# Kernel tuning notes

Measured on AMD Instinct MI355X. Metric: run time of the kernel, lower is better.

## Reference

```python
import jax, jax.numpy as jnp
import numpy as np

PAD_TOKEN = 1
V_EN = 32000
V_DE = 32000
WORD_DIM = 300
HID = 500
VLAYER = 500


def lstm(x, Wih, Whh, bih, bhh):
    """Single-layer batch-first LSTM, PyTorch gate order (i,f,g,o). x: [B,T,D] -> h: [B,T,H]."""
    xg = jnp.einsum('btd,gd->btg', x, Wih) + bih  # precompute input projections [B,T,4H]
    H = Whh.shape[1]
    B = x.shape[0]

    def step(carry, xg_t):
        h, c = carry
        g = xg_t + h @ Whh.T + bhh
        i, f, gg, o = jnp.split(g, 4, axis=-1)
        c = jax.nn.sigmoid(f) * c + jax.nn.sigmoid(i) * jnp.tanh(gg)
        h = jax.nn.sigmoid(o) * jnp.tanh(c)
        return (h, c), h

    h0 = jnp.zeros((B, H), x.dtype)
    (_, _), hs = jax.lax.scan(step, (h0, h0), jnp.swapaxes(xg, 0, 1))
    return jnp.swapaxes(hs, 0, 1)


def setup_inputs() -> dict:
    key = jax.random.key(0)
    ks = jax.random.split(key, 12)
    B, S, T = 64, 50, 50
    s = 0.05
    inp = {
        'x_de': jax.random.randint(ks[0], (B, S), 0, V_DE),
        'x_en': jax.random.randint(ks[1], (B, T), 0, V_EN),
        'emb_de_w': jax.random.normal(ks[2], (V_DE, WORD_DIM)) * s,
        'emb_en_w': jax.random.normal(ks[3], (V_EN, WORD_DIM)) * s,
        'enc_Wih': jax.random.normal(ks[4], (4 * HID, WORD_DIM)) * s,
        'enc_Whh': jax.random.normal(ks[5], (4 * HID, HID)) * s,
        'enc_bih': jnp.zeros((4 * HID,)),
        'enc_bhh': jnp.zeros((4 * HID,)),
        'dec_Wih': jax.random.normal(ks[6], (4 * HID, WORD_DIM)) * s,
        'dec_Whh': jax.random.normal(ks[7], (4 * HID, HID)) * s,
        'dec_bih': jnp.zeros((4 * HID,)),
        'dec_bhh': jnp.zeros((4 * HID,)),
        'h2e_w': jax.random.normal(ks[8], (VLAYER, 2 * HID)) * s,
        'h2e_b': jnp.zeros((VLAYER,)),
        'e2v_w': jax.random.normal(ks[9], (V_EN, VLAYER)) * s,
        'e2v_b': jnp.zeros((V_EN,)),
    }
    return inp


def reference(x_de, x_en, emb_de_w, emb_en_w,
              enc_Wih, enc_Whh, enc_bih, enc_bhh,
              dec_Wih, dec_Whh, dec_bih, dec_bhh,
              h2e_w, h2e_b, e2v_w, e2v_b):
    emb_de = emb_de_w[x_de]                       # [B,S,D]
    emb_en = emb_en_w[x_en]                       # [B,T,D]
    enc_h = lstm(emb_de, enc_Wih, enc_Whh, enc_bih, enc_bhh)  # [B,S,H]
    dec_h = lstm(emb_en, dec_Wih, dec_Whh, dec_bih, dec_bhh)  # [B,T,H]

    Tm1 = dec_h.shape[1] - 1
    scores = jnp.einsum('bsh,bth->bst', enc_h, dec_h[:, :Tm1])  # [B,S,T']

    # hard attention: categorical sample per (b,t), all timesteps vectorized
    logp_attn = jax.nn.log_softmax(scores, axis=1)               # [B,S,T']
    samples = jax.random.categorical(jax.random.key(42),
                                     jnp.swapaxes(scores, 1, 2), axis=-1)  # [B,T'] int
    context = jnp.take_along_axis(enc_h, samples[:, :, None], axis=1)      # [B,T',H]

    feat = jnp.concatenate([dec_h[:, :Tm1], context], axis=-1)   # [B,T',2H]
    e = jnp.tanh(feat @ h2e_w.T + h2e_b)
    pred = jax.nn.log_softmax(e @ e2v_w.T + e2v_b, axis=-1)      # [B,T',V]

    y = x_en[:, 1:]                                              # [B,T']
    mask = (y != PAD_TOKEN).astype(pred.dtype)
    reward = jnp.take_along_axis(pred, y[:, :, None], axis=-1)[..., 0]  # [B,T']
    cnt = jnp.maximum(mask.sum(0), 1.0)

    loss = -jnp.sum((reward * mask).sum(0) / cnt)

    logp_s = jnp.take_along_axis(jnp.swapaxes(logp_attn, 1, 2),
                                 samples[:, :, None], axis=-1)[..., 0]  # [B,T']
    baseline = jnp.log(1.0 / V_EN)
    adv = jax.lax.stop_gradient(reward - baseline)
    reinforce_loss = -jnp.sum((logp_s * adv * mask).sum(0) / cnt)

    return loss, reinforce_loss
```

## Files before the change

kernel.cpp:

```cpp
#include <hip/hip_runtime.h>
#include <cstdint>

typedef short short8 __attribute__((ext_vector_type(8)));
typedef float f32x4 __attribute__((ext_vector_type(4)));
typedef uint32_t u32x4 __attribute__((ext_vector_type(4)));
typedef unsigned short u16;
typedef unsigned long long u64;

__device__ __forceinline__ u16 f2bf(float f) {
  union { float f; uint32_t u; } v; v.f = f;
  uint32_t u = v.u;
  uint32_t r = (u + 0x7fffu + ((u >> 16) & 1u)) >> 16;
  return (u16)r;
}
__device__ __forceinline__ float bf2f(u16 b) {
  union { uint32_t u; float f; } v; v.u = ((uint32_t)b) << 16; return v.f;
}
__device__ __forceinline__ float sigm(float x) { return 1.f / (1.f + expf(-x)); }
__device__ __forceinline__ float tanh_f(float x) { return 2.f / (1.f + expf(-2.f * x)) - 1.f; }

typedef const __attribute__((address_space(1))) uint32_t glb_u32;
typedef __attribute__((address_space(3))) uint32_t lds_u32;
__device__ __forceinline__ void glds16(const void* g, void* l) {
  __builtin_amdgcn_global_load_lds((glb_u32*)g, (lds_u32*)l, 16, 0, 0);
}

__device__ __forceinline__ void tfround(uint32_t& a, uint32_t& b, int r) {
  a += b; b = (b << r) | (b >> (32 - r)); b ^= a;
}
__device__ __forceinline__ void threefry(uint32_t k0, uint32_t k1, uint32_t& x0, uint32_t& x1) {
  uint32_t k2 = k0 ^ k1 ^ 0x1BD11BDAu;
  x0 += k0; x1 += k1;
  tfround(x0,x1,13); tfround(x0,x1,15); tfround(x0,x1,26); tfround(x0,x1,6);
  x0 += k1; x1 += k2 + 1u;
  tfround(x0,x1,17); tfround(x0,x1,29); tfround(x0,x1,16); tfround(x0,x1,24);
  x0 += k2; x1 += k0 + 2u;
  tfround(x0,x1,13); tfround(x0,x1,15); tfround(x0,x1,26); tfround(x0,x1,6);
  x0 += k0; x1 += k1 + 3u;
  tfround(x0,x1,17); tfround(x0,x1,29); tfround(x0,x1,16); tfround(x0,x1,24);
  x0 += k1; x1 += k2 + 4u;
  tfround(x0,x1,13); tfround(x0,x1,15); tfround(x0,x1,26); tfround(x0,x1,6);
  x0 += k2; x1 += k0 + 5u;
}
__device__ __forceinline__ float gumbel_from_bits(uint32_t bits) {
  float f = __uint_as_float((bits >> 9) | 0x3f800000u) - 1.0f;
  const float tiny = 1.17549435e-38f;
  float u = fmaxf(f + tiny, tiny);
  return -logf(-logf(u));
}

__global__ __launch_bounds__(256) void prep_all(
    const float* eWih, const float* eWhh, const float* ebih, const float* ebhh,
    const float* dWih, const float* dWhh, const float* dbih, const float* dbhh,
    const float* h2e_w, const float* h2e_b, const float* e2v_w,
    u16* wih_p, u16* whh_p, float* bsum, u16* h2e_p, float* h2e_bp,
    u16* e2v_p, u16* hglob, int* bar)
{
  const uint32_t GWIH = 2u*2048u*40u;
  const uint32_t GWHH = 2u*2048u*64u;
  const uint32_t GBS  = 512u;
  const uint32_t GH2E = 512u*128u;
  const uint32_t GH2EB= 64u;
  const uint32_t GE2V = 32000u*64u;
  const uint32_t GHG  = 16384u;
  const uint32_t GBAR = 64u;
  const uint32_t TOT  = GWIH+GWHH+GBS+GH2E+GH2EB+GE2V+GHG+GBAR;
  for (uint32_t i = blockIdx.x*256u + threadIdx.x; i < TOT; i += gridDim.x*256u) {
    uint32_t j = i;
    if (j < GWIH) {
      uint32_t L = j / (2048u*40u), rem = j % (2048u*40u);
      uint32_t p = rem / 40u, kg = rem % 40u;
      uint32_t g = p >> 9, u = p & 511u, k0 = kg*8u;
      short8 o = {0,0,0,0,0,0,0,0}; u16* op = (u16*)&o;
      if (u < 500u) {
        const float* src = (L ? dWih : eWih) + ((size_t)(g*500u+u))*300u + k0;
        if (k0 + 8u <= 300u) {
          float4 a = *(const float4*)src, b = *(const float4*)(src+4);
          op[0]=f2bf(a.x);op[1]=f2bf(a.y);op[2]=f2bf(a.z);op[3]=f2bf(a.w);
          op[4]=f2bf(b.x);op[5]=f2bf(b.y);op[6]=f2bf(b.z);op[7]=f2bf(b.w);
        } else {
          #pragma unroll
          for (int e = 0; e < 8; ++e) if (k0+e < 300u) op[e] = f2bf(src[e]);
        }
      }
      *(short8*)(wih_p + (size_t)j*8) = o; continue;
    }
    j -= GWIH;
    if (j < GWHH) {
      uint32_t L = j / (2048u*64u), rem = j % (2048u*64u);
      uint32_t row = rem >> 6, kg = rem & 63u, k0 = kg*8u;
      uint32_t wg = row >> 7, r2 = row & 127u, g = r2 >> 5, ul = r2 & 31u;
      uint32_t u = wg*32u + ul;
      short8 o = {0,0,0,0,0,0,0,0}; u16* op = (u16*)&o;
      if (u < 500u) {
        const float* src = (L ? dWhh : eWhh) + ((size_t)(g*500u+u))*500u + k0;
        if (k0 + 8u <= 500u) {
          float4 a = *(const float4*)src, b = *(const float4*)(src+4);
          op[0]=f2bf(a.x);op[1]=f2bf(a.y);op[2]=f2bf(a.z);op[3]=f2bf(a.w);
          op[4]=f2bf(b.x);op[5]=f2bf(b.y);op[6]=f2bf(b.z);op[7]=f2bf(b.w);
        } else {
          #pragma unroll
          for (int e = 0; e < 8; ++e) if (k0+e < 500u) op[e] = f2bf(src[e]);
        }
      }
      *(short8*)(whh_p + (size_t)j*8) = o; continue;
    }
    j -= GWHH;
    if (j < GBS) {
      uint32_t L = j >> 8, pg = j & 255u, p0 = pg*8u;
      float arr[8];
      #pragma unroll
      for (int e = 0; e < 8; ++e) {
        uint32_t p = p0 + e, g = p >> 9, u = p & 511u;
        arr[e] = (u < 500u) ? ((L?dbih:ebih)[g*500u+u] + (L?dbhh:ebhh)[g*500u+u]) : 0.f;
      }
      *(float4*)(bsum + (size_t)j*8) = *(float4*)arr;
      *(float4*)(bsum + (size_t)j*8 + 4) = *(float4*)(arr+4);
      continue;
    }
    j -= GBS;
    if (j < GH2E) {
      uint32_t n = j >> 7, kg = j & 127u, k0 = kg*8u;
      short8 o = {0,0,0,0,0,0,0,0}; u16* op = (u16*)&o;
      if (n < 500u) {
        const float* rowp = h2e_w + (size_t)n*1000u;
        if (k0 + 8u <= 500u) {
          float4 a = *(const float4*)(rowp+k0), b = *(const float4*)(rowp+k0+4);
          op[0]=f2bf(a.x);op[1]=f2bf(a.y);op[2]=f2bf(a.z);op[3]=f2bf(a.w);
          op[4]=f2bf(b.x);op[5]=f2bf(b.y);op[6]=f2bf(b.z);op[7]=f2bf(b.w);
        } else if (k0 >= 512u && k0 + 8u <= 1012u) {
          #pragma unroll
          for (int e = 0; e < 8; ++e) op[e] = f2bf(rowp[k0 + e - 12u]);
        } else {
          #pragma unroll
          for (int e = 0; e < 8; ++e) {
            uint32_t k = k0 + e; float v = 0.f;
            if (k < 500u) v = rowp[k];
            else if (k >= 512u && k < 1012u) v = rowp[k - 12u];
            op[e] = f2bf(v);
          }
        }
      }
      *(short8*)(h2e_p + (size_t)j*8) = o; continue;
    }
    j -= GH2E;
    if (j < GH2EB) {
      uint32_t k0 = j*8u;
      float arr[8];
      #pragma unroll
      for (int e = 0; e < 8; ++e) { uint32_t k = k0+e; arr[e] = (k < 500u) ? h2e_b[k] : 0.f; }
      *(float4*)(h2e_bp + (size_t)j*8) = *(float4*)arr;
      *(float4*)(h2e_bp + (size_t)j*8 + 4) = *(float4*)(arr+4);
      continue;
    }
    j -= GH2EB;
    if (j < GE2V) {
      uint32_t n = j >> 6, kg = j & 63u, k0 = kg*8u;
      short8 o = {0,0,0,0,0,0,0,0}; u16* op = (u16*)&o;
      const float* src = e2v_w + (size_t)n*500u + k0;
      if (k0 + 8u <= 500u) {
        float4 a = *(const float4*)src, b = *(const float4*)(src+4);
        op[0]=f2bf(a.x);op[1]=f2bf(a.y);op[2]=f2bf(a.z);op[3]=f2bf(a.w);
        op[4]=f2bf(b.x);op[5]=f2bf(b.y);op[6]=f2bf(b.z);op[7]=f2bf(b.w);
      } else {
        #pragma unroll
        for (int e = 0; e < 8; ++e) if (k0+e < 500u) op[e] = f2bf(src[e]);
      }
      *(short8*)(e2v_p + (size_t)j*8) = o; continue;
    }
    j -= GE2V;
    if (j < GHG) { short8 z = {0,0,0,0,0,0,0,0}; *(short8*)(hglob + (size_t)j*8) = z; continue; }
    j -= GHG;
    if (j < GBAR) bar[j] = 0;
  }
}

__global__ __launch_bounds__(256, 1) void lstm_kernel(
    const u16* xg , const u16* whh_p,
    u16* hglob , float* h_out , int* bar)
{
  const int wg = blockIdx.x;
  const int lstm = wg >> 4;
  const int wgl = wg & 15;
  const int tid = threadIdx.x;
  const int wid = tid >> 6;
  const int lane = tid & 63;

  __shared__ u16 hbuf[64 * 512];
  __shared__ float pre[4][64][34];
  __shared__ u16 hsh[64 * 32];

  short8 wf[2][16];
  {
    const u16* wbase = whh_p + ((size_t)lstm*2048 + wgl*128 + wid*32) * 512;
    #pragma unroll
    for (int nt = 0; nt < 2; ++nt)
      #pragma unroll
      for (int kk = 0; kk < 16; ++kk) {
        int row = nt*16 + (lane & 15);
        int k = kk*32 + (lane >> 4)*8;
        wf[nt][kk] = *(const short8*)(wbase + (size_t)row*512 + k);
      }
  }

  float c[8];
  #pragma unroll
  for (int q = 0; q < 8; ++q) c[q] = 0.f;

  int* mybar = bar + lstm*32;
  const int ug = wgl*32 + (tid & 31);
  const u16* xgl = xg + ((size_t)lstm*3200)*2048;

  float xr[4][8];
  #pragma unroll
  for (int q = 0; q < 8; ++q) {
    int b = q*8 + (tid >> 5);
    size_t xrow = ((size_t)(b*50 + 0))*2048;
    #pragma unroll
    for (int g = 0; g < 4; ++g) xr[g][q] = bf2f(xgl[xrow + g*512 + ug]);
  }

  #pragma unroll 1
  for (int t = 0; t < 50; ++t) {
    const int cur = t & 1;
    {
      u32x4 sv[16];
      const char* sbase = (const char*)(hglob + ((size_t)(cur*2 + lstm))*64*512);
      #pragma unroll
      for (int i = 0; i < 16; ++i) {
        const void* p = sbase + (size_t)(i*256 + tid)*16;
        asm volatile("global_load_dwordx4 %0, %1, off sc0 sc1" : "=v"(sv[i]) : "v"(p));
      }
      asm volatile("s_waitcnt vmcnt(0)" ::: "memory");
      __builtin_amdgcn_sched_barrier(0);
      #pragma unroll
      for (int i = 0; i < 16; ++i) {
        int chunk = i*256 + tid;
        int row = chunk >> 6, col16 = chunk & 63;
        int byte = row*1024 + ((col16*16) ^ ((row & 7) << 4));
        *(u32x4*)((char*)hbuf + byte) = sv[i];
      }
    }
    __syncthreads();

    f32x4 zero = {0.f, 0.f, 0.f, 0.f};
    f32x4 acc[4][2];
    #pragma unroll
    for (int m = 0; m < 4; ++m) { acc[m][0] = zero; acc[m][1] = zero; }

    #pragma unroll
    for (int kk = 0; kk < 16; ++kk) {
      short8 af[4];
      #pragma unroll
      for (int m = 0; m < 4; ++m) {
        int row = m*16 + (lane & 15);
        int byte = row*1024 + ((kk*64 + (lane >> 4)*16) ^ ((row & 7) << 4));
        af[m] = *(const short8*)((const char*)hbuf + byte);
      }
      #pragma unroll
      for (int m = 0; m < 4; ++m) {
        acc[m][0] = __builtin_amdgcn_mfma_f32_16x16x32_bf16(af[m], wf[0][kk], acc[m][0], 0, 0, 0);
        acc[m][1] = __builtin_amdgcn_mfma_f32_16x16x32_bf16(af[m], wf[1][kk], acc[m][1], 0, 0, 0);
      }
    }

    #pragma unroll
    for (int m = 0; m < 4; ++m)
      #pragma unroll
      for (int nt = 0; nt < 2; ++nt)
        #pragma unroll
        for (int jj = 0; jj < 4; ++jj) {
          int row = m*16 + (lane >> 4)*4 + jj;
          int col = nt*16 + (lane & 15);
          pre[wid][row][col] = acc[m][nt][jj];
        }
    __syncthreads();

    #pragma unroll
    for (int q = 0; q < 8; ++q) {
      int b = q*8 + (tid >> 5);
      int ul = tid & 31;
      float pi = pre[0][b][ul] + xr[0][q];
      float pf = pre[1][b][ul] + xr[1][q];
      float pg = pre[2][b][ul] + xr[2][q];
      float po = pre[3][b][ul] + xr[3][q];
      c[q] = sigm(pf)*c[q] + sigm(pi)*tanh_f(pg);
      float h = sigm(po)*tanh_f(c[q]);
      if (ug >= 500) h = 0.f;
      h_out[(((size_t)(lstm*64 + b))*50 + t)*512 + ug] = h;
      hsh[b*32 + ul] = f2bf(h);
    }
    if (t == 49) break;
    __syncthreads();

    {
      u16* hdst = hglob + ((size_t)((cur^1)*2 + lstm))*64*512;
      int b2 = tid >> 2, c8 = (tid & 3)*8;
      u32x4 w = *(const u32x4*)(hsh + b2*32 + c8);
      void* dp = hdst + (size_t)b2*512 + wgl*32 + c8;
      asm volatile("global_store_dwordx4 %0, %1, off sc0 sc1" :: "v"(dp), "v"(w) : "memory");
    }
    asm volatile("s_waitcnt vmcnt(0)" ::: "memory");

    if (tid == 0)
      __hip_atomic_fetch_add(mybar, 1, __ATOMIC_RELAXED, __HIP_MEMORY_SCOPE_AGENT);

    {
      const int tn = t + 1;
      #pragma unroll
      for (int q = 0; q < 8; ++q) {
        int b = q*8 + (tid >> 5);
        size_t xrow = ((size_t)(b*50 + tn))*2048;
        #pragma unroll
        for (int g = 0; g < 4; ++g) xr[g][q] = bf2f(xgl[xrow + g*512 + ug]);
      }
    }

    if (tid == 0) {
      int target = 16*(t+1);
      while (__hip_atomic_load(mybar, __ATOMIC_RELAXED, __HIP_MEMORY_SCOPE_AGENT) < target) {}
    }
    __syncthreads();
  }
}

__global__ __launch_bounds__(256) void scores_kernel(const float* h_out, float* scores) {
  int b = blockIdx.x >> 2, tq = blockIdx.x & 3;
  int tid = threadIdx.x, wid = tid >> 6, lane = tid & 63;
  __shared__ float enc[50*512];
  const float* ebase = h_out + ((size_t)b*50)*512;
  for (int i = tid*4; i < 50*512; i += 256*4)
    *(float4*)(enc + i) = *(const float4*)(ebase + i);
  __syncthreads();
  const int t0 = tq*13;
  const int cnt = (tq == 3) ? 10 : 13;
  for (int tl = wid; tl < cnt; tl += 4) {
    int t = t0 + tl;
    const float* drow = h_out + ((size_t)((64 + b)*50 + t))*512;
    float d[8];
    #pragma unroll
    for (int j = 0; j < 8; ++j) d[j] = drow[lane + j*64];
    for (int s = 0; s < 50; ++s) {
      float p = 0.f;
      #pragma unroll
      for (int j = 0; j < 8; ++j) p += enc[s*512 + lane + j*64] * d[j];
      #pragma unroll
      for (int mk = 32; mk; mk >>= 1) p += __shfl_xor(p, mk);
      if (lane == 0) scores[((size_t)(b*50 + s))*49 + t] = p;
    }
  }
}

__global__ __launch_bounds__(256) void sample_kernel(const float* scores, int* samples, float* logp_s) {
  int p = blockIdx.x*4 + (threadIdx.x >> 6);
  int lane = threadIdx.x & 63;
  int b = p / 49, t = p - b*49;
  float sc = -INFINITY;
  if (lane < 50) sc = scores[((size_t)(b*50 + lane))*49 + t];
  float val = -INFINITY;
  if (lane < 50) {
    uint32_t i = (uint32_t)(p*50 + lane);
    uint32_t x0, x1; int sel;
    if (i < 78400u) { x0 = i; x1 = i + 78400u; sel = 0; }
    else            { x0 = i - 78400u; x1 = i; sel = 1; }
    threefry(0u, 42u, x0, x1);
    val = sc + gumbel_from_bits(sel ? x1 : x0);
  }
  int idx = lane; float v = val;
  #pragma unroll
  for (int mk = 1; mk < 64; mk <<= 1) {
    float ov = __shfl_xor(v, mk);
    int oi = __shfl_xor(idx, mk);
    if (ov > v || (ov == v && oi < idx)) { v = ov; idx = oi; }
  }
  float m = sc;
  #pragma unroll
  for (int mk = 1; mk < 64; mk <<= 1) m = fmaxf(m, __shfl_xor(m, mk));
  float e = (lane < 50) ? expf(sc - m) : 0.f;
  #pragma unroll
  for (int mk = 1; mk < 64; mk <<= 1) e += __shfl_xor(e, mk);
  float lse = m + logf(e);
  float scs = __shfl(sc, idx);
  if (lane == 0) { samples[p] = idx; logp_s[p] = scs - lse; }
}

template <int AMODE, int EPI>
__global__ __launch_bounds__(256) void gemm_k(
    const float* Af32a, const float* Af32b, const int* gia, const int* gib,
    const u16* Abf, const u16* Bp, int ldkB, int KT,
    float* Cf32, u16* Cbf, const float* bias,
    float* pm, float* ps, float* ylogit)
{
  int Mb, Nb;
  if constexpr (EPI == 2) {
    int bid = blockIdx.y*gridDim.x + blockIdx.x;
    const int NBLK = 25*250, q = NBLK/8, r = NBLK%8;
    int xcd = bid & 7, idx = bid >> 3;
    int wgid = (xcd < r ? xcd*(q+1) : r*(q+1) + (xcd-r)*q) + idx;
    Mb = wgid % 25; Nb = wgid / 25;
  } else { Mb = blockIdx.x; Nb = blockIdx.y; }
  const int zb = blockIdx.z;
  const int tid = threadIdx.x;
  const int wid = tid >> 6, lane = tid & 63;
  const int wr = wid >> 1, wc = wid & 1;

  __shared__ u16 As[2*128*64];
  __shared__ u16 Bs[2*128*64];
  __shared__ float part[128][2][2];

  f32x4 zero = {0.f,0.f,0.f,0.f};
  f32x4 acc[4][4];
  #pragma unroll
  for (int m = 0; m < 4; ++m)
    #pragma unroll
    for (int n = 0; n < 4; ++n) acc[m][n] = zero;

  auto MFMA_STEP = [&](int buf) {
    #pragma unroll
    for (int kk2 = 0; kk2 < 2; ++kk2) {
      short8 a[4], b[4];
      #pragma unroll
      for (int m = 0; m < 4; ++m) {
        int row = wr*64 + m*16 + (lane & 15);
        int byte = buf*16384 + row*128 + ((kk2*64 + (lane >> 4)*16) ^ ((row & 7) << 4));
        a[m] = *(const short8*)((const char*)As + byte);
      }
      #pragma unroll
      for (int n = 0; n < 4; ++n) {
        int row = wc*64 + n*16 + (lane & 15);
        int byte = buf*16384 + row*128 + ((kk2*64 + (lane >> 4)*16) ^ ((row & 7) << 4));
        b[n] = *(const short8*)((const char*)Bs + byte);
      }
      #pragma unroll
      for (int m = 0; m < 4; ++m)
        #pragma unroll
        for (int n = 0; n < 4; ++n)
          acc[m][n] = __builtin_amdgcn_mfma_f32_16x16x32_bf16(a[m], b[n], acc[m][n], 0, 0, 0);
    }
  };

  if constexpr (AMODE == 2) {
    auto ISSUE = [&](int it, int buf) {
      #pragma unroll
      for (int i = 0; i < 4; ++i) {
        int chunk = i*256 + tid;
        int row = chunk >> 3, c16 = chunk & 7;
        int cg = c16 ^ (row & 7);
        const u16* sa = Abf + (size_t)(Mb*128 + row)*512 + it*64 + cg*8;
        const u16* sb = Bp  + (size_t)(Nb*128 + row)*512 + it*64 + cg*8;
        char* da = (char*)As + buf*16384 + i*4096 + wid*1024;
        char* db = (char*)Bs + buf*16384 + i*4096 + wid*1024;
        glds16(sa, da);
        glds16(sb, db);
      }
    };
    ISSUE(0, 0);
    asm volatile("s_waitcnt vmcnt(0)" ::: "memory");
    __syncthreads();
    for (int it = 0; it < KT; ++it) {
      const int buf = it & 1;
      if (it + 1 < KT) ISSUE(it + 1, buf ^ 1);
      MFMA_STEP(buf);
      if (it + 1 < KT) {
        asm volatile("s_waitcnt vmcnt(0)" ::: "memory");
        __syncthreads();
      }
    }
  } else {
    const int r = tid >> 1;
    const int koff = (tid & 1)*32;
    const int growA = Mb*128 + r;
    const int growB = Nb*128 + r;

    const float* emb = nullptr; const int* ids = nullptr;
    int fb = 0, ft = 0, fsmp = 0; bool fvalid = true;
    if constexpr (AMODE == 0) {
      emb = zb ? Af32b : Af32a;
      ids = zb ? gib : gia;
    } else {
      fvalid = growA < 3136;
      fb = growA / 49; ft = growA - fb*49;
      fsmp = fvalid ? gia[growA] : 0;
    }

    short8 av8[4], bv8[4];
    auto FETCH = [&](int it) {
      const int k0 = it*64 + koff;
      u16* avp = (u16*)av8;
      if constexpr (AMODE == 0) {
        const float* srow = emb + (size_t)ids[growA]*300;
        #pragma unroll
        for (int j = 0; j < 8; ++j) {
          int k = k0 + j*4;
          float4 v = make_float4(0.f,0.f,0.f,0.f);
          if (k + 4 <= 300) v = *(const float4*)(srow + k);
          avp[j*4+0]=f2bf(v.x); avp[j*4+1]=f2bf(v.y); avp[j*4+2]=f2bf(v.z); avp[j*4+3]=f2bf(v.w);
        }
      } else {
        #pragma unroll
        for (int j = 0; j < 8; ++j) {
          int k = k0 + j*4;
          float4 v = make_float4(0.f,0.f,0.f,0.f);
          if (fvalid) {
            if (k + 4 <= 500) v = *(const float4*)(Af32a + ((size_t)(fb*50 + ft))*512 + k);
            else if (k >= 512 && k + 4 <= 1012) v = *(const float4*)(Af32b + ((size_t)(fb*50 + fsmp))*512 + (k - 512));
          }
          avp[j*4+0]=f2bf(v.x); avp[j*4+1]=f2bf(v.y); avp[j*4+2]=f2bf(v.z); avp[j*4+3]=f2bf(v.w);
        }
      }
      #pragma unroll
      for (int j = 0; j < 4; ++j)
        bv8[j] = *(const short8*)(Bp + (size_t)growB*ldkB + k0 + j*8);
    };
    auto STORE_LDS = [&](int buf) {
      #pragma unroll
      for (int j = 0; j < 4; ++j) {
        int byte = buf*16384 + r*128 + ((koff*2 + j*16) ^ ((r & 7) << 4));
        *(short8*)((char*)As + byte) = av8[j];
        *(short8*)((char*)Bs + byte) = bv8[j];
      }
    };

    FETCH(0);
    STORE_LDS(0);
    __syncthreads();
    for (int it = 0; it < KT; ++it) {
      const int cur = it & 1;
      if (it + 1 < KT) FETCH(it + 1);
      MFMA_STEP(cur);
      __syncthreads();
      if (it + 1 < KT) {
        STORE_LDS(cur ^ 1);
        __syncthreads();
      }
    }
  }

  if constexpr (EPI == 0) {
    u16* C = Cbf + (size_t)zb*3200*2048;
    const float* bs = bias + (size_t)zb*2048;
    #pragma unroll
    for (int m = 0; m < 4; ++m)
      #pragma unroll
      for (int n = 0; n < 4; ++n)
        #pragma unroll
        for (int jj = 0; jj < 4; ++jj) {
          int row = Mb*128 + wr*64 + m*16 + (lane >> 4)*4 + jj;
          int col = Nb*128 + wc*64 + n*16 + (lane & 15);
          C[(size_t)row*2048 + col] = f2bf(acc[m][n][jj] + bs[col]);
        }
  } else if constexpr (EPI == 1) {
    #pragma unroll
    for (int m = 0; m < 4; ++m)
      #pragma unroll
      for (int n = 0; n < 4; ++n)
        #pragma unroll
        for (int jj = 0; jj < 4; ++jj) {
          int row = Mb*128 + wr*64 + m*16 + (lane >> 4)*4 + jj;
          int col = Nb*128 + wc*64 + n*16 + (lane & 15);
          float e = tanh_f(acc[m][n][jj] + bias[col]);
          Cbf[(size_t)row*512 + col] = f2bf(e);
        }
  } else {
    float bias4[4];
    #pragma unroll
    for (int n = 0; n < 4; ++n) bias4[n] = bias[Nb*128 + wc*64 + n*16 + (lane & 15)];
    #pragma unroll
    for (int m = 0; m < 4; ++m)
      #pragma unroll
      for (int jj = 0; jj < 4; ++jj) {
        int trow = wr*64 + m*16 + (lane >> 4)*4 + jj;
        int grow = Mb*128 + trow;
        float x0 = acc[m][0][jj] + bias4[0];
        float x1 = acc[m][1][jj] + bias4[1];
        float x2 = acc[m][2][jj] + bias4[2];
        float x3 = acc[m][3][jj] + bias4[3];
        float mx = fmaxf(fmaxf(x0,x1), fmaxf(x2,x3));
        #pragma unroll
        for (int mk = 1; mk < 16; mk <<= 1) mx = fmaxf(mx, __shfl_xor(mx, mk));
        float sm = expf(x0-mx) + expf(x1-mx) + expf(x2-mx) + expf(x3-mx);
        #pragma unroll
        for (int mk = 1; mk < 16; mk <<= 1) sm += __shfl_xor(sm, mk);
        if (grow < 3136) {
          int b = grow / 49, tt = grow - b*49;
          int yv = gib[b*50 + tt + 1];
          int cb = yv - (Nb*128 + wc*64);
          if (cb == 0*16 + (lane & 15)) ylogit[grow] = x0;
          if (cb == 1*16 + (lane & 15)) ylogit[grow] = x1;
          if (cb == 2*16 + (lane & 15)) ylogit[grow] = x2;
          if (cb == 3*16 + (lane & 15)) ylogit[grow] = x3;
        }
        if ((lane & 15) == 0) { part[trow][wc][0] = mx; part[trow][wc][1] = sm; }
      }
    __syncthreads();
    if (tid < 128) {
      int grow = Mb*128 + tid;
      if (grow < 3136) {
        float m0 = part[tid][0][0], s0 = part[tid][0][1];
        float m1 = part[tid][1][0], s1 = part[tid][1][1];
        float M = fmaxf(m0, m1);
        float S = s0*expf(m0 - M) + s1*expf(m1 - M);
        pm[(size_t)grow*250 + Nb] = M;
        ps[(size_t)grow*250 + Nb] = S;
      }
    }
  }
}

__global__ __launch_bounds__(256) void lse_reduce(const float* pm, const float* ps,
                                                  const float* ylogit, float* reward) {
  int row = blockIdx.x*4 + (threadIdx.x >> 6);
  int lane = threadIdx.x & 63;
  if (row >= 3136) return;
  float M = -INFINITY, S = 0.f;
  for (int j = lane; j < 250; j += 64) {
    float m = pm[(size_t)row*250 + j], s = ps[(size_t)row*250 + j];
    float nm = fmaxf(M, m);
    S = S*expf(M - nm) + s*expf(m - nm);
    M = nm;
  }
  #pragma unroll
  for (int mk = 1; mk < 64; mk <<= 1) {
    float om = __shfl_xor(M, mk), os = __shfl_xor(S, mk);
    float nm = fmaxf(M, om);
    S = S*expf(M - nm) + os*expf(om - nm);
    M = nm;
  }
  if (lane == 0) reward[row] = ylogit[row] - (M + logf(S));
}

__global__ void final_kernel(const float* reward, const float* logp_s, const int* x_en, float* out) {
  int t = threadIdx.x;
  float tl = 0.f, trl = 0.f;
  const float baseline = logf(1.0f / 32000.0f);
  if (t < 49) {
    float sr = 0.f, srl = 0.f; int cm = 0;
    for (int b = 0; b < 64; ++b) {
      int yv = x_en[b*50 + t + 1];
      if (yv != 1) {
        float rw = reward[b*49 + t];
        sr += rw;
        srl += logp_s[b*49 + t] * (rw - baseline);
        cm += 1;
      }
    }
    float cnt = fmaxf((float)cm, 1.f);
    tl = sr / cnt; trl = srl / cnt;
  }
  #pragma unroll
  for (int mk = 1; mk < 64; mk <<= 1) { tl += __shfl_xor(tl, mk); trl += __shfl_xor(trl, mk); }
  if (t == 0) { out[0] = -tl; out[1] = -trl; }
}

extern "C" void kernel_launch(void* const* d_in, const int* in_sizes, int n_in,
                              void* d_out, int out_size, void* d_ws, size_t ws_size,
                              hipStream_t stream) {
  (void)in_sizes; (void)n_in; (void)out_size; (void)ws_size;
  const int*   x_de    = (const int*)d_in[0];
  const int*   x_en    = (const int*)d_in[1];
  const float* emb_de  = (const float*)d_in[2];
  const float* emb_en  = (const float*)d_in[3];
  const float* enc_Wih = (const float*)d_in[4];
  const float* enc_Whh = (const float*)d_in[5];
  const float* enc_bih = (const float*)d_in[6];
  const float* enc_bhh = (const float*)d_in[7];
  const float* dec_Wih = (const float*)d_in[8];
  const float* dec_Whh = (const float*)d_in[9];
  const float* dec_bih = (const float*)d_in[10];
  const float* dec_bhh = (const float*)d_in[11];
  const float* h2e_w   = (const float*)d_in[12];
  const float* h2e_b   = (const float*)d_in[13];
  const float* e2v_w   = (const float*)d_in[14];
  const float* e2v_b   = (const float*)d_in[15];
  float* out = (float*)d_out;

  char* ws = (char*)d_ws;
  size_t o = 0;
  auto alloc = [&](size_t bytes) { size_t rr = o; o += (bytes + 255) & ~(size_t)255; return rr; };
  int*   bar     = (int*)  (ws + alloc(256));
  u16*   wih_p   = (u16*)  (ws + alloc(2ull*2048*320*2));
  u16*   whh_p   = (u16*)  (ws + alloc(2ull*2048*512*2));
  float* bsum    = (float*)(ws + alloc(2ull*2048*4));
  u16*   h2e_p   = (u16*)  (ws + alloc(512ull*1024*2));
  float* h2e_bp  = (float*)(ws + alloc(512ull*4));
  u16*   e2v_p   = (u16*)  (ws + alloc(32000ull*512*2));
  u16*   xg      = (u16*)  (ws + alloc(2ull*3200*2048*2));
  u16*   hglob   = (u16*)  (ws + alloc(2ull*2*64*512*2));
  float* h_out   = (float*)(ws + alloc(2ull*64*50*512*4));
  float* scores  = (float*)(ws + alloc(64ull*50*49*4));
  int*   samples = (int*)  (ws + alloc(3136ull*4));
  float* logp_s  = (float*)(ws + alloc(3136ull*4));
  float* ylogit  = (float*)(ws + alloc(3200ull*4));
  float* reward  = (float*)(ws + alloc(3136ull*4));
  u16*   e_buf   = (u16*)  (ws + alloc(3200ull*512*2));
  float* pmb     = (float*)(ws + alloc(3200ull*250*4));
  float* psb     = (float*)(ws + alloc(3200ull*250*4));

  prep_all<<<2048, 256, 0, stream>>>(enc_Wih, enc_Whh, enc_bih, enc_bhh,
      dec_Wih, dec_Whh, dec_bih, dec_bhh, h2e_w, h2e_b, e2v_w,
      wih_p, whh_p, bsum, h2e_p, h2e_bp, e2v_p, hglob, bar);

  gemm_k<0,0><<<dim3(25,16,2), 256, 0, stream>>>(emb_de, emb_en, x_de, x_en,
      nullptr, wih_p, 320, 5, nullptr, xg, bsum, nullptr, nullptr, nullptr);

  lstm_kernel<<<32, 256, 0, stream>>>(xg, whh_p, hglob, h_out, bar);

  scores_kernel<<<256, 256, 0, stream>>>(h_out, scores);

  sample_kernel<<<784, 256, 0, stream>>>(scores, samples, logp_s);

  gemm_k<1,1><<<dim3(25,4,1), 256, 0, stream>>>(h_out + 64ull*50*512, h_out, samples, nullptr,
      nullptr, h2e_p, 1024, 16, nullptr, e_buf, h2e_bp, nullptr, nullptr, nullptr);

  gemm_k<2,2><<<dim3(25,250,1), 256, 0, stream>>>(nullptr, nullptr, nullptr, x_en,
      e_buf, e2v_p, 512, 8, nullptr, nullptr, e2v_b, pmb, psb, ylogit);

  lse_reduce<<<784, 256, 0, stream>>>(pmb, psb, ylogit, reward);

  final_kernel<<<1, 64, 0, stream>>>(reward, logp_s, x_en, out);
}
```

Baseline: 815.6 us.

## Replace LSTM atomic counter barrier with per-block flags; add B-stationary vocab GEMM

The LSTM grid barrier moves from one shared atomic counter to per-workgroup step flags on separate cache lines. One wave polls all 16 flags and exits via ballot, which removes contention on a single atomic. The vocab projection GEMM becomes a dedicated kernel with 250 persistent blocks. Each block keeps its full 128x512 e2v weight tile resident in LDS (128 KB) and streams all 25 row tiles of activations, so weights are read once instead of per M-tile. The cost is one block per CU and more serial work per block.

```diff
diff --git a/kernel.cpp b/kernel.cpp
--- a/kernel.cpp
+++ b/kernel.cpp
@@ -63,7 +63,7 @@
   const uint32_t GH2EB= 64u;
   const uint32_t GE2V = 32000u*64u;
   const uint32_t GHG  = 16384u;
-  const uint32_t GBAR = 64u;
+  const uint32_t GBAR = 512u;
   const uint32_t TOT  = GWIH+GWHH+GBS+GH2E+GH2EB+GE2V+GHG+GBAR;
   for (uint32_t i = blockIdx.x*256u + threadIdx.x; i < TOT; i += gridDim.x*256u) {
     uint32_t j = i;
@@ -207,7 +207,7 @@
   #pragma unroll
   for (int q = 0; q < 8; ++q) c[q] = 0.f;
 
-  int* mybar = bar + lstm*32;
+  int* flags = bar + lstm*256;
   const int ug = wgl*32 + (tid & 31);
   const u16* xgl = xg + ((size_t)lstm*3200)*2048;
 
@@ -301,9 +301,10 @@
       asm volatile("global_store_dwordx4 %0, %1, off sc0 sc1" :: "v"(dp), "v"(w) : "memory");
     }
     asm volatile("s_waitcnt vmcnt(0)" ::: "memory");
+    __syncthreads();
 
     if (tid == 0)
-      __hip_atomic_fetch_add(mybar, 1, __ATOMIC_RELAXED, __HIP_MEMORY_SCOPE_AGENT);
+      __hip_atomic_store(flags + wgl*16, t+1, __ATOMIC_RELAXED, __HIP_MEMORY_SCOPE_AGENT);
 
     {
       const int tn = t + 1;
@@ -316,9 +317,12 @@
       }
     }
 
-    if (tid == 0) {
-      int target = 16*(t+1);
-      while (__hip_atomic_load(mybar, __ATOMIC_RELAXED, __HIP_MEMORY_SCOPE_AGENT) < target) {}
+    if (wid == 0) {
+      int fj = (lane & 15) * 16;
+      while (true) {
+        int v = __hip_atomic_load(flags + fj, __ATOMIC_RELAXED, __HIP_MEMORY_SCOPE_AGENT);
+        if (__ballot(v >= t + 1) == ~0ull) break;
+      }
     }
     __syncthreads();
   }
@@ -391,22 +395,13 @@
     float* Cf32, u16* Cbf, const float* bias,
     float* pm, float* ps, float* ylogit)
 {
-  int Mb, Nb;
-  if constexpr (EPI == 2) {
-    int bid = blockIdx.y*gridDim.x + blockIdx.x;
-    const int NBLK = 25*250, q = NBLK/8, r = NBLK%8;
-    int xcd = bid & 7, idx = bid >> 3;
-    int wgid = (xcd < r ? xcd*(q+1) : r*(q+1) + (xcd-r)*q) + idx;
-    Mb = wgid % 25; Nb = wgid / 25;
-  } else { Mb = blockIdx.x; Nb = blockIdx.y; }
-  const int zb = blockIdx.z;
+  const int Mb = blockIdx.x, Nb = blockIdx.y, zb = blockIdx.z;
   const int tid = threadIdx.x;
   const int wid = tid >> 6, lane = tid & 63;
   const int wr = wid >> 1, wc = wid & 1;
 
   __shared__ u16 As[2*128*64];
   __shared__ u16 Bs[2*128*64];
-  __shared__ float part[128][2][2];
 
   f32x4 zero = {0.f,0.f,0.f,0.f};
   f32x4 acc[4][4];
@@ -439,100 +434,71 @@
     }
   };
 
-  if constexpr (AMODE == 2) {
-    auto ISSUE = [&](int it, int buf) {
-      #pragma unroll
-      for (int i = 0; i < 4; ++i) {
-        int chunk = i*256 + tid;
-        int row = chunk >> 3, c16 = chunk & 7;
-        int cg = c16 ^ (row & 7);
-        const u16* sa = Abf + (size_t)(Mb*128 + row)*512 + it*64 + cg*8;
-        const u16* sb = Bp  + (size_t)(Nb*128 + row)*512 + it*64 + cg*8;
-        char* da = (char*)As + buf*16384 + i*4096 + wid*1024;
-        char* db = (char*)Bs + buf*16384 + i*4096 + wid*1024;
-        glds16(sa, da);
-        glds16(sb, db);
-      }
-    };
-    ISSUE(0, 0);
-    asm volatile("s_waitcnt vmcnt(0)" ::: "memory");
+  const int r = tid >> 1;
+  const int koff = (tid & 1)*32;
+  const int growA = Mb*128 + r;
+  const int growB = Nb*128 + r;
+
+  const float* emb = nullptr; const int* ids = nullptr;
+  int fb = 0, ft = 0, fsmp = 0; bool fvalid = true;
+  if constexpr (AMODE == 0) {
+    emb = zb ? Af32b : Af32a;
+    ids = zb ? gib : gia;
+  } else {
+    fvalid = growA < 3136;
+    fb = growA / 49; ft = growA - fb*49;
+    fsmp = fvalid ? gia[growA] : 0;
+  }
+
+  short8 av8[4], bv8[4];
+  auto FETCH = [&](int it) {
+    const int k0 = it*64 + koff;
+    u16* avp = (u16*)av8;
+    if constexpr (AMODE == 0) {
+      const float* srow = emb + (size_t)ids[growA]*300;
+      #pragma unroll
+      for (int j = 0; j < 8; ++j) {
+        int k = k0 + j*4;
+        float4 v = make_float4(0.f,0.f,0.f,0.f);
+        if (k + 4 <= 300) v = *(const float4*)(srow + k);
+        avp[j*4+0]=f2bf(v.x); avp[j*4+1]=f2bf(v.y); avp[j*4+2]=f2bf(v.z); avp[j*4+3]=f2bf(v.w);
+      }
+    } else {
+      #pragma unroll
+      for (int j = 0; j < 8; ++j) {
+        int k = k0 + j*4;
+        float4 v = make_float4(0.f,0.f,0.f,0.f);
+        if (fvalid) {
+          if (k + 4 <= 500) v = *(const float4*)(Af32a + ((size_t)(fb*50 + ft))*512 + k);
+          else if (k >= 512 && k + 4 <= 1012) v = *(const float4*)(Af32b + ((size_t)(fb*50 + fsmp))*512 + (k - 512));
+        }
+        avp[j*4+0]=f2bf(v.x); avp[j*4+1]=f2bf(v.y); avp[j*4+2]=f2bf(v.z); avp[j*4+3]=f2bf(v.w);
+      }
+    }
+    #pragma unroll
+    for (int j = 0; j < 4; ++j)
+      bv8[j] = *(const short8*)(Bp + (size_t)growB*ldkB + k0 + j*8);
+  };
+  auto STORE_LDS = [&](int buf) {
+    #pragma unroll
+    for (int j = 0; j < 4; ++j) {
+      int byte = buf*16384 + r*128 + ((koff*2 + j*16) ^ ((r & 7) << 4));
+      *(short8*)((char*)As + byte) = av8[j];
+      *(short8*)((char*)Bs + byte) = bv8[j];
+    }
+  };
+
+  FETCH(0);
+  STORE_LDS(0);
+  __syncthreads();
+  for (int it = 0; it < KT; ++it) {
+    const int cur = it & 1;
+    if (it + 1 < KT) FETCH(it + 1);
+    MFMA_STEP(cur);
     __syncthreads();
-    for (int it = 0; it < KT; ++it) {
-      const int buf = it & 1;
-      if (it + 1 < KT) ISSUE(it + 1, buf ^ 1);
-      MFMA_STEP(buf);
-      if (it + 1 < KT) {
-        asm volatile("s_waitcnt vmcnt(0)" ::: "memory");
-        __syncthreads();
-      }
-    }
-  } else {
-    const int r = tid >> 1;
-    const int koff = (tid & 1)*32;
-    const int growA = Mb*128 + r;
-    const int growB = Nb*128 + r;
-
-    const float* emb = nullptr; const int* ids = nullptr;
-    int fb = 0, ft = 0, fsmp = 0; bool fvalid = true;
-    if constexpr (AMODE == 0) {
-      emb = zb ? Af32b : Af32a;
-      ids = zb ? gib : gia;
-    } else {
-      fvalid = growA < 3136;
-      fb = growA / 49; ft = growA - fb*49;
-      fsmp = fvalid ? gia[growA] : 0;
-    }
-
-    short8 av8[4], bv8[4];
-    auto FETCH = [&](int it) {
-      const int k0 = it*64 + koff;
-      u16* avp = (u16*)av8;
-      if constexpr (AMODE == 0) {
-        const float* srow = emb + (size_t)ids[growA]*300;
-        #pragma unroll
-        for (int j = 0; j < 8; ++j) {
-          int k = k0 + j*4;
-          float4 v = make_float4(0.f,0.f,0.f,0.f);
-          if (k + 4 <= 300) v = *(const float4*)(srow + k);
-          avp[j*4+0]=f2bf(v.x); avp[j*4+1]=f2bf(v.y); avp[j*4+2]=f2bf(v.z); avp[j*4+3]=f2bf(v.w);
-        }
-      } else {
-        #pragma unroll
-        for (int j = 0; j < 8; ++j) {
-          int k = k0 + j*4;
-          float4 v = make_float4(0.f,0.f,0.f,0.f);
-          if (fvalid) {
-            if (k + 4 <= 500) v = *(const float4*)(Af32a + ((size_t)(fb*50 + ft))*512 + k);
-            else if (k >= 512 && k + 4 <= 1012) v = *(const float4*)(Af32b + ((size_t)(fb*50 + fsmp))*512 + (k - 512));
-          }
-          avp[j*4+0]=f2bf(v.x); avp[j*4+1]=f2bf(v.y); avp[j*4+2]=f2bf(v.z); avp[j*4+3]=f2bf(v.w);
-        }
-      }
-      #pragma unroll
-      for (int j = 0; j < 4; ++j)
-        bv8[j] = *(const short8*)(Bp + (size_t)growB*ldkB + k0 + j*8);
-    };
-    auto STORE_LDS = [&](int buf) {
-      #pragma unroll
-      for (int j = 0; j < 4; ++j) {
-        int byte = buf*16384 + r*128 + ((koff*2 + j*16) ^ ((r & 7) << 4));
-        *(short8*)((char*)As + byte) = av8[j];
-        *(short8*)((char*)Bs + byte) = bv8[j];
-      }
-    };
-
-    FETCH(0);
-    STORE_LDS(0);
-    __syncthreads();
-    for (int it = 0; it < KT; ++it) {
-      const int cur = it & 1;
-      if (it + 1 < KT) FETCH(it + 1);
-      MFMA_STEP(cur);
+    if (it + 1 < KT) {
+      STORE_LDS(cur ^ 1);
       __syncthreads();
-      if (it + 1 < KT) {
-        STORE_LDS(cur ^ 1);
-        __syncthreads();
-      }
     }
   }
 
@@ -549,7 +515,7 @@
           int col = Nb*128 + wc*64 + n*16 + (lane & 15);
           C[(size_t)row*2048 + col] = f2bf(acc[m][n][jj] + bs[col]);
         }
-  } else if constexpr (EPI == 1) {
+  } else {
     #pragma unroll
     for (int m = 0; m < 4; ++m)
       #pragma unroll
@@ -561,16 +527,98 @@
           float e = tanh_f(acc[m][n][jj] + bias[col]);
           Cbf[(size_t)row*512 + col] = f2bf(e);
         }
-  } else {
-    float bias4[4];
-    #pragma unroll
-    for (int n = 0; n < 4; ++n) bias4[n] = bias[Nb*128 + wc*64 + n*16 + (lane & 15)];
+  }
+}
+
+__global__ __launch_bounds__(256, 1) void gemm_e2v(
+    const u16* e_buf, const u16* e2v_p, const int* x_en, const float* bias,
+    float* pm, float* ps, float* ylogit)
+{
+  const int tid = threadIdx.x;
+  const int wid = tid >> 6, lane = tid & 63;
+  const int wr = wid >> 1, wc = wid & 1;
+
+  int bid = blockIdx.x;
+  const int q = 250/8, r = 250%8;
+  int xcd = bid & 7, idx = bid >> 3;
+  int Nb = (xcd < r ? xcd*(q+1) : r*(q+1) + (xcd-r)*q) + idx;
+
+  __shared__ u16 Bs[128*512];
+  __shared__ u16 As[2][128*32];
+  __shared__ float part[128][2][2];
+
+  #pragma unroll 4
+  for (int i = 0; i < 32; ++i) {
+    int chunk = i*256 + tid;
+    int row = chunk >> 6, c = chunk & 63;
+    int cg = c ^ (row & 7);
+    const u16* src = e2v_p + (size_t)(Nb*128 + row)*512 + cg*8;
+    char* dst = (char*)Bs + (size_t)(i*256 + wid*64)*16;
+    glds16(src, dst);
+  }
+
+  auto ISSUE_A = [&](int mt, int kt, int buf) {
+    #pragma unroll
+    for (int i = 0; i < 2; ++i) {
+      int chunk = i*256 + tid;
+      int row = chunk >> 2, c = chunk & 3;
+      int cg = c ^ (row & 3);
+      const u16* src = e_buf + (size_t)(mt*128 + row)*512 + kt*32 + cg*8;
+      char* dst = (char*)(&As[buf][0]) + (size_t)(i*256 + wid*64)*16;
+      glds16(src, dst);
+    }
+  };
+
+  ISSUE_A(0, 0, 0);
+  asm volatile("s_waitcnt vmcnt(0)" ::: "memory");
+  __syncthreads();
+
+  float bias4[4];
+  #pragma unroll
+  for (int n = 0; n < 4; ++n) bias4[n] = bias[Nb*128 + wc*64 + n*16 + (lane & 15)];
+
+  for (int mt = 0; mt < 25; ++mt) {
+    f32x4 zero = {0.f,0.f,0.f,0.f};
+    f32x4 acc[4][4];
+    #pragma unroll
+    for (int m = 0; m < 4; ++m)
+      #pragma unroll
+      for (int n = 0; n < 4; ++n) acc[m][n] = zero;
+
+    for (int kt = 0; kt < 16; ++kt) {
+      const int buf = kt & 1;
+      if (kt + 1 < 16)      ISSUE_A(mt, kt + 1, buf ^ 1);
+      else if (mt + 1 < 25) ISSUE_A(mt + 1, 0, buf ^ 1);
+
+      short8 a[4], b[4];
+      #pragma unroll
+      for (int m = 0; m < 4; ++m) {
+        int row = wr*64 + m*16 + (lane & 15);
+        int byte = row*64 + (((lane >> 4)*16) ^ ((row & 3) << 4));
+        a[m] = *(const short8*)((const char*)(&As[buf][0]) + byte);
+      }
+      #pragma unroll
+      for (int n = 0; n < 4; ++n) {
+        int row = wc*64 + n*16 + (lane & 15);
+        int byte = row*1024 + ((kt*64 + (lane >> 4)*16) ^ ((row & 7) << 4));
+        b[n] = *(const short8*)((const char*)Bs + byte);
+      }
+      #pragma unroll
+      for (int m = 0; m < 4; ++m)
+        #pragma unroll
+        for (int n = 0; n < 4; ++n)
+          acc[m][n] = __builtin_amdgcn_mfma_f32_16x16x32_bf16(a[m], b[n], acc[m][n], 0, 0, 0);
+
+      asm volatile("s_waitcnt vmcnt(0)" ::: "memory");
+      __syncthreads();
+    }
+
     #pragma unroll
     for (int m = 0; m < 4; ++m)
       #pragma unroll
       for (int jj = 0; jj < 4; ++jj) {
         int trow = wr*64 + m*16 + (lane >> 4)*4 + jj;
-        int grow = Mb*128 + trow;
+        int grow = mt*128 + trow;
         float x0 = acc[m][0][jj] + bias4[0];
         float x1 = acc[m][1][jj] + bias4[1];
         float x2 = acc[m][2][jj] + bias4[2];
@@ -583,7 +631,7 @@
         for (int mk = 1; mk < 16; mk <<= 1) sm += __shfl_xor(sm, mk);
         if (grow < 3136) {
           int b = grow / 49, tt = grow - b*49;
-          int yv = gib[b*50 + tt + 1];
+          int yv = x_en[b*50 + tt + 1];
           int cb = yv - (Nb*128 + wc*64);
           if (cb == 0*16 + (lane & 15)) ylogit[grow] = x0;
           if (cb == 1*16 + (lane & 15)) ylogit[grow] = x1;
@@ -594,7 +642,7 @@
       }
     __syncthreads();
     if (tid < 128) {
-      int grow = Mb*128 + tid;
+      int grow = mt*128 + tid;
       if (grow < 3136) {
         float m0 = part[tid][0][0], s0 = part[tid][0][1];
         float m1 = part[tid][1][0], s1 = part[tid][1][1];
@@ -604,6 +652,7 @@
         ps[(size_t)grow*250 + Nb] = S;
       }
     }
+    __syncthreads();
   }
 }
 
@@ -677,7 +726,7 @@
   char* ws = (char*)d_ws;
   size_t o = 0;
   auto alloc = [&](size_t bytes) { size_t rr = o; o += (bytes + 255) & ~(size_t)255; return rr; };
-  int*   bar     = (int*)  (ws + alloc(256));
+  int*   bar     = (int*)  (ws + alloc(2048));
   u16*   wih_p   = (u16*)  (ws + alloc(2ull*2048*320*2));
   u16*   whh_p   = (u16*)  (ws + alloc(2ull*2048*512*2));
   float* bsum    = (float*)(ws + alloc(2ull*2048*4));
@@ -712,8 +761,7 @@
   gemm_k<1,1><<<dim3(25,4,1), 256, 0, stream>>>(h_out + 64ull*50*512, h_out, samples, nullptr,
       nullptr, h2e_p, 1024, 16, nullptr, e_buf, h2e_bp, nullptr, nullptr, nullptr);
 
-  gemm_k<2,2><<<dim3(25,250,1), 256, 0, stream>>>(nullptr, nullptr, nullptr, x_en,
-      e_buf, e2v_p, 512, 8, nullptr, nullptr, e2v_b, pmb, psb, ylogit);
+  gemm_e2v<<<250, 256, 0, stream>>>(e_buf, e2v_p, x_en, e2v_b, pmb, psb, ylogit);
 
   lse_reduce<<<784, 256, 0, stream>>>(pmb, psb, ylogit, reward);
 
```

Result: slower. 988.1 us (+21.2%).

## Replace atomic counter barrier with per-block flags and fuse scores with sampling

Applied to the files above, without the earlier changes.

The LSTM grid barrier no longer has every block doing an atomic add on one shared counter. Each block now stores its step number into its own padded flag slot, and one wavefront polls all 16 flags with a ballot, which removes the contention on a single atomic. The scores and Gumbel-sampling kernels are merged so each wave keeps its 50 scores in lanes and samples directly. That drops one launch and the global round trip through a scores buffer. An extra __syncthreads is added before the flag store so all threads' hidden-state stores complete before the flag is published.

```diff
diff --git a/kernel.cpp b/kernel.cpp
--- a/kernel.cpp
+++ b/kernel.cpp
@@ -63,7 +63,7 @@
   const uint32_t GH2EB= 64u;
   const uint32_t GE2V = 32000u*64u;
   const uint32_t GHG  = 16384u;
-  const uint32_t GBAR = 64u;
+  const uint32_t GBAR = 512u;
   const uint32_t TOT  = GWIH+GWHH+GBS+GH2E+GH2EB+GE2V+GHG+GBAR;
   for (uint32_t i = blockIdx.x*256u + threadIdx.x; i < TOT; i += gridDim.x*256u) {
     uint32_t j = i;
@@ -207,7 +207,7 @@
   #pragma unroll
   for (int q = 0; q < 8; ++q) c[q] = 0.f;
 
-  int* mybar = bar + lstm*32;
+  int* flags = bar + lstm*256;
   const int ug = wgl*32 + (tid & 31);
   const u16* xgl = xg + ((size_t)lstm*3200)*2048;
 
@@ -301,9 +301,10 @@
       asm volatile("global_store_dwordx4 %0, %1, off sc0 sc1" :: "v"(dp), "v"(w) : "memory");
     }
     asm volatile("s_waitcnt vmcnt(0)" ::: "memory");
+    __syncthreads();
 
     if (tid == 0)
-      __hip_atomic_fetch_add(mybar, 1, __ATOMIC_RELAXED, __HIP_MEMORY_SCOPE_AGENT);
+      __hip_atomic_store(flags + wgl*16, t+1, __ATOMIC_RELAXED, __HIP_MEMORY_SCOPE_AGENT);
 
     {
       const int tn = t + 1;
@@ -316,15 +317,19 @@
       }
     }
 
-    if (tid == 0) {
-      int target = 16*(t+1);
-      while (__hip_atomic_load(mybar, __ATOMIC_RELAXED, __HIP_MEMORY_SCOPE_AGENT) < target) {}
+    if (wid == 0) {
+      int fj = (lane & 15) * 16;
+      while (true) {
+        int v = __hip_atomic_load(flags + fj, __ATOMIC_RELAXED, __HIP_MEMORY_SCOPE_AGENT);
+        if (__ballot(v >= t + 1) == ~0ull) break;
+      }
     }
     __syncthreads();
   }
 }
 
-__global__ __launch_bounds__(256) void scores_kernel(const float* h_out, float* scores) {
+__global__ __launch_bounds__(256) void scores_sample_kernel(const float* h_out,
+                                                            int* samples, float* logp_s) {
   int b = blockIdx.x >> 2, tq = blockIdx.x & 3;
   int tid = threadIdx.x, wid = tid >> 6, lane = tid & 63;
   __shared__ float enc[50*512];
@@ -340,48 +345,42 @@
     float d[8];
     #pragma unroll
     for (int j = 0; j < 8; ++j) d[j] = drow[lane + j*64];
+    float sc = -INFINITY;
     for (int s = 0; s < 50; ++s) {
       float p = 0.f;
       #pragma unroll
       for (int j = 0; j < 8; ++j) p += enc[s*512 + lane + j*64] * d[j];
       #pragma unroll
       for (int mk = 32; mk; mk >>= 1) p += __shfl_xor(p, mk);
-      if (lane == 0) scores[((size_t)(b*50 + s))*49 + t] = p;
-    }
-  }
-}
-
-__global__ __launch_bounds__(256) void sample_kernel(const float* scores, int* samples, float* logp_s) {
-  int p = blockIdx.x*4 + (threadIdx.x >> 6);
-  int lane = threadIdx.x & 63;
-  int b = p / 49, t = p - b*49;
-  float sc = -INFINITY;
-  if (lane < 50) sc = scores[((size_t)(b*50 + lane))*49 + t];
-  float val = -INFINITY;
-  if (lane < 50) {
-    uint32_t i = (uint32_t)(p*50 + lane);
-    uint32_t x0, x1; int sel;
-    if (i < 78400u) { x0 = i; x1 = i + 78400u; sel = 0; }
-    else            { x0 = i - 78400u; x1 = i; sel = 1; }
-    threefry(0u, 42u, x0, x1);
-    val = sc + gumbel_from_bits(sel ? x1 : x0);
-  }
-  int idx = lane; float v = val;
-  #pragma unroll
-  for (int mk = 1; mk < 64; mk <<= 1) {
-    float ov = __shfl_xor(v, mk);
-    int oi = __shfl_xor(idx, mk);
-    if (ov > v || (ov == v && oi < idx)) { v = ov; idx = oi; }
-  }
-  float m = sc;
-  #pragma unroll
-  for (int mk = 1; mk < 64; mk <<= 1) m = fmaxf(m, __shfl_xor(m, mk));
-  float e = (lane < 50) ? expf(sc - m) : 0.f;
-  #pragma unroll
-  for (int mk = 1; mk < 64; mk <<= 1) e += __shfl_xor(e, mk);
-  float lse = m + logf(e);
-  float scs = __shfl(sc, idx);
-  if (lane == 0) { samples[p] = idx; logp_s[p] = scs - lse; }
+      if (lane == s) sc = p;
+    }
+    const int pidx = b*49 + t;
+    float val = -INFINITY;
+    if (lane < 50) {
+      uint32_t i = (uint32_t)(pidx*50 + lane);
+      uint32_t x0, x1; int sel;
+      if (i < 78400u) { x0 = i; x1 = i + 78400u; sel = 0; }
+      else            { x0 = i - 78400u; x1 = i; sel = 1; }
+      threefry(0u, 42u, x0, x1);
+      val = sc + gumbel_from_bits(sel ? x1 : x0);
+    }
+    int idx = lane; float v = val;
+    #pragma unroll
+    for (int mk = 1; mk < 64; mk <<= 1) {
+      float ov = __shfl_xor(v, mk);
+      int oi = __shfl_xor(idx, mk);
+      if (ov > v || (ov == v && oi < idx)) { v = ov; idx = oi; }
+    }
+    float m = sc;
+    #pragma unroll
+    for (int mk = 1; mk < 64; mk <<= 1) m = fmaxf(m, __shfl_xor(m, mk));
+    float e = (lane < 50) ? expf(sc - m) : 0.f;
+    #pragma unroll
+    for (int mk = 1; mk < 64; mk <<= 1) e += __shfl_xor(e, mk);
+    float lse = m + logf(e);
+    float scs = __shfl(sc, idx);
+    if (lane == 0) { samples[pidx] = idx; logp_s[pidx] = scs - lse; }
+  }
 }
 
 template <int AMODE, int EPI>
@@ -677,7 +676,7 @@
   char* ws = (char*)d_ws;
   size_t o = 0;
   auto alloc = [&](size_t bytes) { size_t rr = o; o += (bytes + 255) & ~(size_t)255; return rr; };
-  int*   bar     = (int*)  (ws + alloc(256));
+  int*   bar     = (int*)  (ws + alloc(2048));
   u16*   wih_p   = (u16*)  (ws + alloc(2ull*2048*320*2));
   u16*   whh_p   = (u16*)  (ws + alloc(2ull*2048*512*2));
   float* bsum    = (float*)(ws + alloc(2ull*2048*4));
@@ -687,7 +686,6 @@
   u16*   xg      = (u16*)  (ws + alloc(2ull*3200*2048*2));
   u16*   hglob   = (u16*)  (ws + alloc(2ull*2*64*512*2));
   float* h_out   = (float*)(ws + alloc(2ull*64*50*512*4));
-  float* scores  = (float*)(ws + alloc(64ull*50*49*4));
   int*   samples = (int*)  (ws + alloc(3136ull*4));
   float* logp_s  = (float*)(ws + alloc(3136ull*4));
   float* ylogit  = (float*)(ws + alloc(3200ull*4));
@@ -705,9 +703,7 @@
 
   lstm_kernel<<<32, 256, 0, stream>>>(xg, whh_p, hglob, h_out, bar);
 
-  scores_kernel<<<256, 256, 0, stream>>>(h_out, scores);
-
-  sample_kernel<<<784, 256, 0, stream>>>(scores, samples, logp_s);
+  scores_sample_kernel<<<256, 256, 0, stream>>>(h_out, samples, logp_s);
 
   gemm_k<1,1><<<dim3(25,4,1), 256, 0, stream>>>(h_out + 64ull*50*512, h_out, samples, nullptr,
       nullptr, h2e_p, 1024, 16, nullptr, e_buf, h2e_bp, nullptr, nullptr, nullptr);
```

Result: faster. 793.9 us (-2.7%).
